# Optimization experiments

Measured on AMD Instinct MI355X. Metric: run time of the kernel, lower is better.

## Reference

```python
import jax, jax.numpy as jnp
import numpy as np

K = 3      # spline order
NUM = 5    # grid intervals


def bspline_basis(x, grid, k=K):
    """Cox-de Boor recursion. x: (B, D); grid: (num+2k+1,) extended knots.
    Returns basis of shape (B, D, num+k)."""
    xe = x[..., None]                                       # (B, D, 1)
    B = ((xe >= grid[:-1]) & (xe < grid[1:])).astype(x.dtype)  # (B, D, num+2k)
    for p in range(1, k + 1):
        left = (xe - grid[:-(p + 1)]) / (grid[p:-1] - grid[:-(p + 1)])
        right = (grid[p + 1:] - xe) / (grid[p + 1:] - grid[1:-p])
        B = left * B[..., :-1] + right * B[..., 1:]
    return B                                                # (B, D, num+k)


def kan_layer(x, grid, coef, sb, sp, mask, bias):
    """phi(x)[b,o] = sum_i mask[o,i]*(sb[o,i]*silu(x[b,i]) + sp[o,i]*sum_c B[b,i,c]*coef[o,i,c]) + bias[o]"""
    Bsp = bspline_basis(x, grid)                            # (B, in, C)
    spline = jnp.einsum('bic,oic->bo', Bsp, coef * (sp * mask)[:, :, None])
    base = jnp.einsum('bi,oi->bo', jax.nn.silu(x), sb * mask)
    return base + spline + bias


def setup_inputs() -> dict:
    key = jax.random.key(0)
    ks = jax.random.split(key, 6)
    Bch, d0, d1, d2 = 8192, 1024, 2048, 1024
    C = NUM + K                                 # 8 spline coeffs per edge
    h = 2.0 / NUM                               # grid_range [-1,1]
    # extended knot vector: k extra knots each side, num+2k+1 = 12 points
    grid = jnp.arange(-K, NUM + K + 1, dtype=jnp.float32) * h - 1.0
    return {
        "x": jax.random.normal(ks[0], (Bch, d0), jnp.float32) * 0.5,
        "coef0": jax.random.normal(ks[1], (d1, d0, C), jnp.float32) * 0.1,
        "sb0": jax.random.normal(ks[2], (d1, d0), jnp.float32) / np.sqrt(d0).astype(np.float32),
        "sp0": jnp.ones((d1, d0), jnp.float32),
        "mask0": jnp.ones((d1, d0), jnp.float32),
        "bias0": jnp.zeros((d1,), jnp.float32),
        "coef1": jax.random.normal(ks[3], (d2, d1, C), jnp.float32) * 0.1,
        "sb1": jax.random.normal(ks[4], (d2, d1), jnp.float32) / np.sqrt(d1).astype(np.float32),
        "sp1": jnp.ones((d2, d1), jnp.float32),
        "mask1": jnp.ones((d2, d1), jnp.float32),
        "bias1": jnp.zeros((d2,), jnp.float32),
        "grid": grid,
    }


def reference(x, coef0, sb0, sp0, mask0, bias0, coef1, sb1, sp1, mask1, bias1, grid):
    h1 = kan_layer(x, grid, coef0, sb0, sp0, mask0, bias0)
    out = kan_layer(h1, grid, coef1, sb1, sp1, mask1, bias1)
    return out
```

## Files before the change

kernel.cpp:

```cpp
#include <hip/hip_runtime.h>
#include <hip/hip_bf16.h>
#include <cstdint>


typedef __attribute__((ext_vector_type(8))) short short8;
typedef __attribute__((ext_vector_type(4))) short short4v;
typedef __attribute__((ext_vector_type(4))) float f32x4;

#define GLD16(gp, lp)                                                          \
  __builtin_amdgcn_global_load_lds(                                           \
      (const __attribute__((address_space(1))) unsigned int*)(gp),             \
      (__attribute__((address_space(3))) unsigned int*)(lp), 16, 0, 0)

__device__ __forceinline__ unsigned short f2bf(float f) {
  __hip_bfloat16 h = __float2bfloat16(f);
  return *reinterpret_cast<unsigned short*>(&h);
}

__device__ __forceinline__ void basis8(float x, float* w, int& j) {
  float u  = (x + 2.2f) * 2.5f;
  float fj = floorf(u);
  j = (int)fj;
  float t  = u - fj;
  float omt = 1.0f - t;
  float t2 = t * t, t3 = t2 * t;
  w[0] = omt * omt * omt * (1.0f / 6.0f);
  w[1] = (3.0f * t3 - 6.0f * t2 + 4.0f) * (1.0f / 6.0f);
  w[2] = (-3.0f * t3 + 3.0f * t2 + 3.0f * t + 1.0f) * (1.0f / 6.0f);
  w[3] = t3 * (1.0f / 6.0f);
}

__global__ void prep_w(const float* __restrict__ coef, const float* __restrict__ sb,
                       const float* __restrict__ sp, const float* __restrict__ mask,
                       __hip_bfloat16* __restrict__ W, int O, int I) {
  long idx = (long)blockIdx.x * blockDim.x + threadIdx.x;
  long total = (long)O * (I >> 2);
  if (idx >= total) return;
  int qtr = I >> 2;
  int iq = (int)(idx % qtr);
  int o  = (int)(idx / qtr);
  int i  = iq << 2;
  size_t oi = (size_t)o * I + i;
  float4 mk4 = *(const float4*)(mask + oi);
  float4 sp4 = *(const float4*)(sp + oi);
  float4 sb4 = *(const float4*)(sb + oi);
  float spm[4] = {sp4.x * mk4.x, sp4.y * mk4.y, sp4.z * mk4.z, sp4.w * mk4.w};
  float cf[4][8];
  const float4* cp = (const float4*)(coef + oi * 8);
#pragma unroll
  for (int e = 0; e < 4; e++) {
    float4 a = cp[e * 2], b = cp[e * 2 + 1];
    cf[e][0] = a.x; cf[e][1] = a.y; cf[e][2] = a.z; cf[e][3] = a.w;
    cf[e][4] = b.x; cf[e][5] = b.y; cf[e][6] = b.z; cf[e][7] = b.w;
  }
  __hip_bfloat16* base = W + (size_t)o * (size_t)(9 * I) + (i >> 6) * 576 + (i & 63);
#pragma unroll
  for (int c = 0; c < 8; c++) {
    short4v pk;
#pragma unroll
    for (int e = 0; e < 4; e++) pk[e] = (short)f2bf(cf[e][c] * spm[e]);
    *(short4v*)(base + c * 64) = pk;
  }
  short4v ps;
  ps[0] = (short)f2bf(sb4.x * mk4.x); ps[1] = (short)f2bf(sb4.y * mk4.y);
  ps[2] = (short)f2bf(sb4.z * mk4.z); ps[3] = (short)f2bf(sb4.w * mk4.w);
  *(short4v*)(base + 8 * 64) = ps;
}

__global__ void expand_aug(const float* __restrict__ src,
                           __hip_bfloat16* __restrict__ aug,
                           long totalOcts, int I) {
  long idx = (long)blockIdx.x * blockDim.x + threadIdx.x;
  if (idx >= totalOcts) return;
  int  oct = I >> 3;
  int  io = (int)(idx % oct);
  long b  = idx / oct;
  int  i  = io << 3;
  const float* sp = src + b * (size_t)I + i;
  float4 xa = *(const float4*)sp;
  float4 xb = *(const float4*)(sp + 4);
  float xv[8] = {xa.x, xa.y, xa.z, xa.w, xb.x, xb.y, xb.z, xb.w};

  float w[8][4], s[8];
  int   j[8];
#pragma unroll
  for (int e = 0; e < 8; e++) {
    float xe = xv[e];
    s[e] = xe / (1.0f + __expf(-xe));
    basis8(xe, w[e], j[e]);
  }
  __hip_bfloat16* base = aug + b * (size_t)(9 * I) + (i >> 6) * 576 + (i & 63);
#pragma unroll
  for (int c = 0; c < 8; c++) {
    short8 pk;
#pragma unroll
    for (int e = 0; e < 8; e++) {
      int d = j[e] - c;
      float v = 0.0f;
      v = (d == 0) ? w[e][3] : v;
      v = (d == 1) ? w[e][2] : v;
      v = (d == 2) ? w[e][1] : v;
      v = (d == 3) ? w[e][0] : v;
      pk[e] = (short)f2bf(v);
    }
    *(short8*)(base + c * 64) = pk;
  }
  short8 ps;
#pragma unroll
  for (int e = 0; e < 8; e++) ps[e] = (short)f2bf(s[e]);
  *(short8*)(base + 8 * 64) = ps;
}

template <int BN>
__global__ __launch_bounds__(512, 4) void gemm128(
    const __hip_bfloat16* __restrict__ A, const __hip_bfloat16* __restrict__ Bw,
    const float* __restrict__ bias, float* __restrict__ Cout, int N, int K) {
  constexpr int WN   = BN / 4;
  constexpr int NREP = BN / 64;
  constexpr int BUFB = 8192 + BN * 64;
  constexpr int L    = 1 + BN / 128;
  __shared__ __attribute__((aligned(16))) char lds[3 * BUFB];

  const int t = threadIdx.x;
  const int w = t >> 6, l = t & 63;
  const int wr = w >> 2, wc = w & 3;
  const int lr = l & 15;
  const int kbs = ((l >> 4) * 16) ^ (((lr >> 1) & 3) << 4);

  unsigned nwg = gridDim.x * gridDim.y;
  unsigned lin = blockIdx.y * gridDim.x + blockIdx.x;
  unsigned swz = (lin & 7) * (nwg >> 3) + (lin >> 3);
  unsigned bx = swz % gridDim.x, by = swz / gridDim.x;
  size_t brow = (size_t)by * 128, bcol = (size_t)bx * BN;

  f32x4 acc[4][NREP];
#pragma unroll
  for (int m = 0; m < 4; m++)
#pragma unroll
    for (int n = 0; n < NREP; n++) acc[m][n] = (f32x4){0.f, 0.f, 0.f, 0.f};

  const int srow  = t >> 2;
  const int scolb = ((t & 3) * 16) ^ (((srow >> 1) & 3) << 4);
  const __hip_bfloat16* gA0 = A + (brow + srow) * (size_t)K + (scolb >> 1);
  const __hip_bfloat16* gB0 = Bw + (bcol + srow) * (size_t)K + (scolb >> 1);
  const __hip_bfloat16* gB1 = gB0 + (size_t)128 * K;

  char* ldsp = (char*)lds;
  const int paOff = (wr * 64 + lr) * 64 + kbs;
  const int pbOff = 8192 + (wc * WN + lr) * 64 + kbs;

  auto STAGE = [&](int kt, int q) {
    char* bp = ldsp + q * BUFB;
    GLD16(gA0 + (kt << 5), bp + w * 1024);
    GLD16(gB0 + (kt << 5), bp + 8192 + w * 1024);
    if constexpr (BN == 256) GLD16(gB1 + (kt << 5), bp + 16384 + w * 1024);
  };
  auto COMPUTE = [&](int q) {
    const char* pa = ldsp + q * BUFB + paOff;
    const char* pb = ldsp + q * BUFB + pbOff;
    short8 bq[NREP], aq[4];
#pragma unroll
    for (int n = 0; n < NREP; n++) bq[n] = *(const short8*)(pb + n * 1024);
#pragma unroll
    for (int m = 0; m < 4; m++) aq[m] = *(const short8*)(pa + m * 1024);
    __builtin_amdgcn_s_setprio(1);
#pragma unroll
    for (int m = 0; m < 4; m++)
#pragma unroll
      for (int n = 0; n < NREP; n++)
        acc[m][n] = __builtin_amdgcn_mfma_f32_16x16x32_bf16(aq[m], bq[n], acc[m][n], 0, 0, 0);
    __builtin_amdgcn_s_setprio(0);
    __builtin_amdgcn_s_barrier();
  };
  auto VM0 = [&]() { asm volatile("s_waitcnt vmcnt(0)" ::: "memory"); };
  auto VML = [&]() {
    if constexpr (BN == 256) asm volatile("s_waitcnt vmcnt(3)" ::: "memory");
    else                     asm volatile("s_waitcnt vmcnt(2)" ::: "memory");
  };
  auto VM2L = [&]() {
    if constexpr (BN == 256) asm volatile("s_waitcnt vmcnt(6)" ::: "memory");
    else                     asm volatile("s_waitcnt vmcnt(4)" ::: "memory");
  };

  const int NT = K >> 5;

  STAGE(0, 0);
  STAGE(1, 1);
  VML();
  __builtin_amdgcn_s_barrier();

  int q0 = 0;
  for (int kt = 0; kt < NT - 2; ++kt) {
    int q2 = q0 + 2; if (q2 >= 3) q2 -= 3;
    STAGE(kt + 2, q2);
    VM2L();
    __builtin_amdgcn_s_barrier();
    COMPUTE(q0);
    q0 = (q0 == 2) ? 0 : q0 + 1;
  }
  VML();
  __builtin_amdgcn_s_barrier();
  COMPUTE(q0);
  q0 = (q0 == 2) ? 0 : q0 + 1;
  VM0();
  __builtin_amdgcn_s_barrier();
  COMPUTE(q0);

  const int orow = (l >> 4) << 2;
#pragma unroll
  for (int n = 0; n < NREP; n++) {
    size_t col = bcol + (size_t)wc * WN + n * 16 + lr;
    float bv = bias[col];
#pragma unroll
    for (int m = 0; m < 4; m++) {
      size_t row = brow + (size_t)wr * 64 + m * 16 + orow;
#pragma unroll
      for (int r = 0; r < 4; r++)
        Cout[(row + r) * (size_t)N + col] = acc[m][n][r] + bv;
    }
  }
}

extern "C" void kernel_launch(void* const* d_in, const int* in_sizes, int n_in,
                              void* d_out, int out_size, void* d_ws, size_t ws_size,
                              hipStream_t stream) {
  const float* x     = (const float*)d_in[0];
  const float* coef0 = (const float*)d_in[1];
  const float* sb0   = (const float*)d_in[2];
  const float* sp0   = (const float*)d_in[3];
  const float* mask0 = (const float*)d_in[4];
  const float* bias0 = (const float*)d_in[5];
  const float* coef1 = (const float*)d_in[6];
  const float* sb1   = (const float*)d_in[7];
  const float* sp1   = (const float*)d_in[8];
  const float* mask1 = (const float*)d_in[9];
  const float* bias1 = (const float*)d_in[10];
  float* out = (float*)d_out;

  const int B = 8192, D0 = 1024, D1 = 2048, D2 = 1024;
  const int K0 = 9 * D0;
  const int K1 = 9 * D1;
  const int CH = 4096;

  char* ws = (char*)d_ws;
  float*          h1  = (float*)ws;
  __hip_bfloat16* W   = (__hip_bfloat16*)(ws + (size_t)67108864);
  __hip_bfloat16* Aug = (__hip_bfloat16*)(ws + (size_t)104857600);

  {
    long nt = (long)D1 * (D0 / 4);
    prep_w<<<(unsigned)((nt + 255) / 256), 256, 0, stream>>>(coef0, sb0, sp0, mask0, W, D1, D0);
    long no = (long)B * (D0 / 8);
    expand_aug<<<(unsigned)((no + 255) / 256), 256, 0, stream>>>(x, Aug, no, D0);
    dim3 g0(D1 / 256, B / 128);
    gemm128<256><<<g0, 512, 0, stream>>>(Aug, W, bias0, h1, D1, K0);
  }

  {
    long nt = (long)D2 * (D1 / 4);
    prep_w<<<(unsigned)((nt + 255) / 256), 256, 0, stream>>>(coef1, sb1, sp1, mask1, W, D2, D1);
    for (int ch = 0; ch < B / CH; ch++) {
      long no = (long)CH * (D1 / 8);
      expand_aug<<<(unsigned)((no + 255) / 256), 256, 0, stream>>>(
          h1 + (size_t)ch * CH * D1, Aug, no, D1);
      dim3 g1(D2 / 128, CH / 128);
      gemm128<128><<<g1, 512, 0, stream>>>(Aug, W, bias1,
                                           out + (size_t)ch * CH * D2, D2, K1);
    }
  }
}
```

Baseline: 793.3 us.

## Merge weight prep with activation expansion and use 128-wide tiles for layer 0

Folds the weight-packing kernel and the activation basis-expansion kernel into one launch per layer, dispatching threads by index range, so fewer kernel launches are needed. Layer 0's GEMM switches from 256-wide to 128-wide N tiles, doubling the number of workgroups. Launch bounds are raised from 4 to 6 waves' worth of occupancy hint, which may push register pressure and cause spills. The second-layer chunk loop is unrolled by hand.

```diff
diff --git a/kernel.cpp b/kernel.cpp
--- a/kernel.cpp
+++ b/kernel.cpp
@@ -30,12 +30,10 @@
   w[3] = t3 * (1.0f / 6.0f);
 }
 
-__global__ void prep_w(const float* __restrict__ coef, const float* __restrict__ sb,
-                       const float* __restrict__ sp, const float* __restrict__ mask,
-                       __hip_bfloat16* __restrict__ W, int O, int I) {
-  long idx = (long)blockIdx.x * blockDim.x + threadIdx.x;
-  long total = (long)O * (I >> 2);
-  if (idx >= total) return;
+__device__ __forceinline__ void prep_w_item(
+    long idx, const float* __restrict__ coef, const float* __restrict__ sb,
+    const float* __restrict__ sp, const float* __restrict__ mask,
+    __hip_bfloat16* __restrict__ W, int I) {
   int qtr = I >> 2;
   int iq = (int)(idx % qtr);
   int o  = (int)(idx / qtr);
@@ -67,11 +65,9 @@
   *(short4v*)(base + 8 * 64) = ps;
 }
 
-__global__ void expand_aug(const float* __restrict__ src,
-                           __hip_bfloat16* __restrict__ aug,
-                           long totalOcts, int I) {
-  long idx = (long)blockIdx.x * blockDim.x + threadIdx.x;
-  if (idx >= totalOcts) return;
+__device__ __forceinline__ void expand_item(
+    long idx, const float* __restrict__ src, __hip_bfloat16* __restrict__ aug,
+    int I) {
   int  oct = I >> 3;
   int  io = (int)(idx % oct);
   long b  = idx / oct;
@@ -111,14 +107,32 @@
   *(short8*)(base + 8 * 64) = ps;
 }
 
+__global__ void prep_merge(
+    const float* __restrict__ coef, const float* __restrict__ sb,
+    const float* __restrict__ sp, const float* __restrict__ mask,
+    __hip_bfloat16* __restrict__ W, int IW, long nW,
+    const float* __restrict__ xsrc, __hip_bfloat16* __restrict__ aug,
+    int IX, long nX) {
+  long idx = (long)blockIdx.x * blockDim.x + threadIdx.x;
+  if (idx < nW)            prep_w_item(idx, coef, sb, sp, mask, W, IW);
+  else if (idx < nW + nX)  expand_item(idx - nW, xsrc, aug, IX);
+}
+
+__global__ void expand_aug(const float* __restrict__ src,
+                           __hip_bfloat16* __restrict__ aug,
+                           long totalOcts, int I) {
+  long idx = (long)blockIdx.x * blockDim.x + threadIdx.x;
+  if (idx >= totalOcts) return;
+  expand_item(idx, src, aug, I);
+}
+
 template <int BN>
-__global__ __launch_bounds__(512, 4) void gemm128(
+__global__ __launch_bounds__(512, 6) void gemm128(
     const __hip_bfloat16* __restrict__ A, const __hip_bfloat16* __restrict__ Bw,
     const float* __restrict__ bias, float* __restrict__ Cout, int N, int K) {
   constexpr int WN   = BN / 4;
   constexpr int NREP = BN / 64;
   constexpr int BUFB = 8192 + BN * 64;
-  constexpr int L    = 1 + BN / 128;
   __shared__ __attribute__((aligned(16))) char lds[3 * BUFB];
 
   const int t = threadIdx.x;
@@ -247,25 +261,29 @@
   __hip_bfloat16* W   = (__hip_bfloat16*)(ws + (size_t)67108864);
   __hip_bfloat16* Aug = (__hip_bfloat16*)(ws + (size_t)104857600);
 
+  const long nW0 = (long)D1 * (D0 / 4);
+  const long nX0 = (long)B * (D0 / 8);
+  const long nW1 = (long)D2 * (D1 / 4);
+  const long nX1 = (long)CH * (D1 / 8);
+
+  prep_merge<<<(unsigned)((nW0 + nX0) / 256), 256, 0, stream>>>(
+      coef0, sb0, sp0, mask0, W, D0, nW0, x, Aug, D0, nX0);
   {
-    long nt = (long)D1 * (D0 / 4);
-    prep_w<<<(unsigned)((nt + 255) / 256), 256, 0, stream>>>(coef0, sb0, sp0, mask0, W, D1, D0);
-    long no = (long)B * (D0 / 8);
-    expand_aug<<<(unsigned)((no + 255) / 256), 256, 0, stream>>>(x, Aug, no, D0);
-    dim3 g0(D1 / 256, B / 128);
-    gemm128<256><<<g0, 512, 0, stream>>>(Aug, W, bias0, h1, D1, K0);
-  }
-
+    dim3 g0(D1 / 128, B / 128);
+    gemm128<128><<<g0, 512, 0, stream>>>(Aug, W, bias0, h1, D1, K0);
+  }
+
+  prep_merge<<<(unsigned)((nW1 + nX1) / 256), 256, 0, stream>>>(
+      coef1, sb1, sp1, mask1, W, D1, nW1, h1, Aug, D1, nX1);
   {
-    long nt = (long)D2 * (D1 / 4);
-    prep_w<<<(unsigned)((nt + 255) / 256), 256, 0, stream>>>(coef1, sb1, sp1, mask1, W, D2, D1);
-    for (int ch = 0; ch < B / CH; ch++) {
-      long no = (long)CH * (D1 / 8);
-      expand_aug<<<(unsigned)((no + 255) / 256), 256, 0, stream>>>(
-          h1 + (size_t)ch * CH * D1, Aug, no, D1);
-      dim3 g1(D2 / 128, CH / 128);
-      gemm128<128><<<g1, 512, 0, stream>>>(Aug, W, bias1,
-                                           out + (size_t)ch * CH * D2, D2, K1);
-    }
-  }
-}
+    dim3 g1(D2 / 128, CH / 128);
+    gemm128<128><<<g1, 512, 0, stream>>>(Aug, W, bias1, out, D2, K1);
+  }
+  expand_aug<<<(unsigned)(nX1 / 256), 256, 0, stream>>>(
+      h1 + (size_t)CH * D1, Aug, nX1, D1);
+  {
+    dim3 g1(D2 / 128, CH / 128);
+    gemm128<128><<<g1, 512, 0, stream>>>(Aug, W, bias1,
+                                         out + (size_t)CH * D2, D2, K1);
+  }
+}
```

After: 859.7 us. +8.4%, slower.
